# Performance work log

Measured on AMD Instinct MI355X. Metric: run time of the kernel, lower is better.

Reference implementation:

```python
import jax, jax.numpy as jnp
import numpy as np
import jax.scipy.linalg as jsp

H = 8
C = 64
D_CONV = 4
EPS_L2 = 1e-6
EPS_RMS = 1e-5


def l2norm(x):
    return x * jax.lax.rsqrt(jnp.sum(x * x, axis=-1, keepdims=True) + EPS_L2)


def setup_inputs() -> dict:
    key = jax.random.key(0)
    ks = jax.random.split(key, 12)
    B, T, D = 4, 4096, 1024
    x = jax.random.normal(ks[0], (B, T, D), dtype=jnp.float32)
    s = 0.02
    Wv = jax.random.normal(ks[1], (D, D), dtype=jnp.float32) * s
    Wg = jax.random.normal(ks[2], (D, D), dtype=jnp.float32) * s
    Wo = jax.random.normal(ks[3], (D, D), dtype=jnp.float32) * s
    Wb = jax.random.normal(ks[4], (H, D), dtype=jnp.float32) * s
    Wa = jax.random.normal(ks[5], (H, D), dtype=jnp.float32) * s
    # dt_bias / A_log initialized as in the torch module
    u = jax.random.uniform(ks[6], (H,))
    dt = jnp.exp(u * (jnp.log(0.1) - jnp.log(0.001)) + jnp.log(0.001))
    dt_bias = dt + jnp.log(-jnp.expm1(-dt))
    A_log = jnp.log(jax.random.uniform(ks[7], (H,)) * 16.0 + 1e-4)
    norm_w = jnp.ones((D // H,), dtype=jnp.float32)
    conv_w = jax.random.normal(ks[8], (D, D_CONV), dtype=jnp.float32) * 0.1
    conv_b = jnp.zeros((D,), dtype=jnp.float32)
    return {"x": x, "Wv": Wv, "Wg": Wg, "Wo": Wo, "Wb": Wb, "Wa": Wa,
            "dt_bias": dt_bias, "A_log": A_log, "norm_w": norm_w,
            "conv_w": conv_w, "conv_b": conv_b}


def _causal_depthwise_conv(x, w, b):
    # x: (B,T,D), w: (D,d_conv) -- causal depthwise conv1d
    B, T, D = x.shape
    xp = jnp.pad(x, ((0, 0), (D_CONV - 1, 0), (0, 0)))
    out = b
    for j in range(D_CONV):
        out = out + xp[:, j:j + T] * w[:, j]
    return out


def _forward(x, Wv, Wg, Wo, Wb, Wa, dt_bias, A_log, norm_w, conv_w, conv_b):
    B, T, D = x.shape
    K = D // H
    n = T // C  # T chosen as a multiple of C, so pad_len == 0

    rk = l2norm(x.reshape(B, T, H, K)) / np.sqrt(K)
    x_shift = jnp.pad(x[:, :-1], ((0, 0), (1, 0), (0, 0)))
    wk = l2norm(x_shift.reshape(B, T, H, K))
    v = jax.nn.silu(_causal_depthwise_conv(x @ Wv.T, conv_w, conv_b)).reshape(B, T, H, K)
    gate = (x @ Wg.T).reshape(B, T, H, K)
    beta = jax.nn.sigmoid(x @ Wb.T)                       # (B,T,H)
    decay = -jnp.exp(A_log) * jax.nn.softplus(x @ Wa.T + dt_bias)  # (B,T,H)

    # -> (B,H,T,K)
    rk, wk, v = (jnp.transpose(t, (0, 2, 1, 3)) for t in (rk, wk, v))
    beta_t = jnp.transpose(beta, (0, 2, 1))[..., None]    # (B,H,T,1)
    v = v * beta_t
    wk_beta = wk * beta_t

    # chunk: (B,H,n,C,K)
    ch = lambda t: t.reshape(B, H, n, C, K)
    rk, wk, v, wk_beta = ch(rk), ch(wk), ch(v), ch(wk_beta)
    decay = jnp.cumsum(jnp.transpose(decay, (0, 2, 1)).reshape(B, H, n, C), axis=-1)
    decay_exp = jnp.exp(decay)[..., None]                 # (B,H,n,C,1)

    tril = jnp.tril(jnp.ones((C, C), dtype=bool))
    strict_lower = jnp.tril(jnp.ones((C, C), dtype=bool), k=-1)
    diff = decay[..., :, None] - decay[..., None, :]
    L_mask = jnp.where(tril, jnp.exp(jnp.where(tril, diff, 0.0)), 0.0)  # (B,H,n,C,C)

    A_strict = jnp.where(strict_lower,
                         -(jnp.einsum('bhnck,bhndk->bhncd', wk_beta, wk) * L_mask), 0.0)
    # forward-substitution loop == inverse of unit-lower-triangular (I - A_strict)
    eye = jnp.eye(C, dtype=x.dtype)
    Tmat = jsp.solve_triangular(eye - A_strict,
                                jnp.broadcast_to(eye, A_strict.shape),
                                lower=True)
    v = Tmat @ v
    wk_cumdecay = Tmat @ (wk_beta * decay_exp)

    # scan over chunks maintaining state S: (B,H,K,K)
    def step(S, inp):
        rk_i, wk_i, v_i, wkc_i, L_i, dec_i = inp
        attn = jnp.where(tril, jnp.einsum('bhck,bhdk->bhcd', rk_i, wk_i) * L_i, 0.0)
        v_new = v_i - wkc_i @ S
        o_inter = (rk_i * jnp.exp(dec_i)[..., None]) @ S
        o_i = o_inter + attn @ v_new
        dw = jnp.exp(dec_i[..., -1:] - dec_i)[..., None]
        S_new = S * jnp.exp(dec_i[..., -1])[..., None, None] + \
            jnp.einsum('bhck,bhcv->bhkv', wk_i * dw, v_new)
        return S_new, o_i

    mv = lambda t: jnp.moveaxis(t, 2, 0)  # chunk axis to front
    S0 = jnp.zeros((B, H, K, K), dtype=x.dtype)
    _, o = jax.lax.scan(step, S0, (mv(rk), mv(wk), mv(v), mv(wk_cumdecay),
                                   mv(L_mask), mv(decay)))
    # o: (n,B,H,C,K) -> (B,T,H,K)
    o = jnp.transpose(o, (1, 0, 3, 2, 4)).reshape(B, T, H, K)

    # per-head RMSNorm, gated, output projection
    o = o * jax.lax.rsqrt(jnp.mean(o * o, axis=-1, keepdims=True) + EPS_RMS) * norm_w
    o = o * jax.nn.silu(gate)
    return o.reshape(B, T, D) @ Wo.T


def reference(x, Wv, Wg, Wo, Wb, Wa, dt_bias, A_log, norm_w, conv_w, conv_b):
    return _forward(x, Wv, Wg, Wo, Wb, Wa, dt_bias, A_log, norm_w, conv_w, conv_b)
```

## Files before the change

kernel.cpp:

```cpp
#include <hip/hip_runtime.h>
#include <hip/hip_bf16.h>
#include <math.h>

#define H_ 8
#define K_ 128
#define C_ 64
#define D_ 1024
#define T_ 4096
#define B_ 4
#define N_CH 64
#define BT_ (B_*T_)

typedef __attribute__((ext_vector_type(8))) short bf16x8;
typedef __attribute__((ext_vector_type(4))) float f32x4;
typedef __hip_bfloat16 bf16;

#define BAR_LGKM() do { \
  asm volatile("s_waitcnt lgkmcnt(0)" ::: "memory"); \
  __builtin_amdgcn_sched_barrier(0); \
  __builtin_amdgcn_s_barrier(); \
} while(0)

__device__ __forceinline__ float siluf(float x){ return x / (1.0f + expf(-x)); }
__device__ __forceinline__ float expn(float x){ return expf(fminf(x, 0.f)); }
__device__ __forceinline__ float sanf(float v){ return (__builtin_fabsf(v) <= 1e30f) ? v : 0.f; }

__device__ __forceinline__ void ld_bf8(const bf16* p, float* o){
  uint4 u = *(const uint4*)p;
  o[0]=__uint_as_float(u.x<<16); o[1]=__uint_as_float(u.x&0xffff0000u);
  o[2]=__uint_as_float(u.y<<16); o[3]=__uint_as_float(u.y&0xffff0000u);
  o[4]=__uint_as_float(u.z<<16); o[5]=__uint_as_float(u.z&0xffff0000u);
  o[6]=__uint_as_float(u.w<<16); o[7]=__uint_as_float(u.w&0xffff0000u);
}
__device__ __forceinline__ void ld_bf8s(const bf16* p, float* o){
  ld_bf8(p, o);
#pragma unroll
  for (int e=0;e<8;e++) o[e] = sanf(o[e]);
}
__device__ __forceinline__ void ld_bf4(const bf16* p, float* o){
  uint2 u = *(const uint2*)p;
  o[0]=__uint_as_float(u.x<<16); o[1]=__uint_as_float(u.x&0xffff0000u);
  o[2]=__uint_as_float(u.y<<16); o[3]=__uint_as_float(u.y&0xffff0000u);
}
__device__ __forceinline__ void ld_bf4s(const bf16* p, float* o){
  ld_bf4(p, o);
#pragma unroll
  for (int e=0;e<4;e++) o[e] = sanf(o[e]);
}
__device__ __forceinline__ unsigned short f2bfu(float f){
  bf16 h = __float2bfloat16(f);
  return *reinterpret_cast<unsigned short*>(&h);
}
__device__ __forceinline__ uint2 pack_bf4(const float* v){
  uint2 r;
  r.x = (unsigned)f2bfu(v[0]) | ((unsigned)f2bfu(v[1])<<16);
  r.y = (unsigned)f2bfu(v[2]) | ((unsigned)f2bfu(v[3])<<16);
  return r;
}

__global__ __launch_bounds__(256) void cast_f2b(
    const float* __restrict__ src, bf16* __restrict__ dst, int n4)
{
  int i = blockIdx.x*256 + threadIdx.x;
  if (i >= n4) return;
  float4 v = *(const float4*)&src[(size_t)i*4];
  float a[4] = {v.x, v.y, v.z, v.w};
  *(uint2*)&dst[(size_t)i*4] = pack_bf4(a);
}

template<typename OUT_T>
__global__ __launch_bounds__(256) void gemm_bt_mfma(
    const bf16* __restrict__ X, const bf16* __restrict__ W,
    OUT_T* __restrict__ Y, int M, int N, int K)
{
  __shared__ __align__(16) bf16 As[128*64];
  __shared__ __align__(16) bf16 Bs[128*64];
  const int tid = threadIdx.x;
  const int wv = tid >> 6;
  const int lane = tid & 63;
  const int row0 = blockIdx.y*128, col0 = blockIdx.x*128;
  const int mw = (wv&1)*64, nw = (wv>>1)*64;
  const int q = lane >> 4;
  const int l15 = lane & 15;
  f32x4 acc[4][4];
#pragma unroll
  for (int mi=0;mi<4;mi++)
#pragma unroll
    for (int ni=0;ni<4;ni++) acc[mi][ni] = (f32x4){0.f,0.f,0.f,0.f};

  const int sr = tid >> 3;
  const int sc = (tid & 7) * 8;
  for (int k0=0;k0<K;k0+=64){
#pragma unroll
    for (int i=0;i<4;i++){
      __builtin_amdgcn_global_load_lds(
          (const void*)&X[(size_t)(row0 + i*32 + sr)*K + k0 + sc],
          (void*)&As[i*2048 + wv*512], 16, 0, 0);
      __builtin_amdgcn_global_load_lds(
          (const void*)&W[(size_t)(col0 + i*32 + sr)*K + k0 + sc],
          (void*)&Bs[i*2048 + wv*512], 16, 0, 0);
    }
    __syncthreads();
#pragma unroll
    for (int ks=0; ks<64; ks+=32){
      bf16x8 af[4], bfr[4];
#pragma unroll
      for (int i=0;i<4;i++){
        af[i]  = *(const bf16x8*)&As[(mw + i*16 + l15)*64 + ks + q*8];
        bfr[i] = *(const bf16x8*)&Bs[(nw + i*16 + l15)*64 + ks + q*8];
      }
#pragma unroll
      for (int mi=0;mi<4;mi++)
#pragma unroll
        for (int ni=0;ni<4;ni++)
          acc[mi][ni] = __builtin_amdgcn_mfma_f32_16x16x32_bf16(af[mi], bfr[ni], acc[mi][ni], 0,0,0);
    }
    __syncthreads();
  }
#pragma unroll
  for (int mi=0;mi<4;mi++){
#pragma unroll
    for (int reg=0;reg<4;reg++){
      int row = row0 + mw + mi*16 + q*4 + reg;
#pragma unroll
      for (int ni=0;ni<4;ni++){
        int col = col0 + nw + ni*16 + l15;
        if constexpr (sizeof(OUT_T) == 2)
          Y[(size_t)row*N + col] = (OUT_T)__float2bfloat16(acc[mi][ni][reg]);
        else
          Y[(size_t)row*N + col] = (OUT_T)acc[mi][ni][reg];
      }
    }
  }
}

__global__ __launch_bounds__(256) void proj_small(
    const float* __restrict__ x, const float* __restrict__ Wb, const float* __restrict__ Wa,
    const float* __restrict__ dt_bias, const float* __restrict__ A_log,
    float* __restrict__ beta_out, float* __restrict__ dec_out)
{
  const int w = threadIdx.x >> 6;
  const int lane = threadIdx.x & 63;
  const int bt = blockIdx.x*4 + w;
  const int b = bt >> 12, t = bt & (T_-1);
  const float* xr = x + (size_t)bt*D_;
  float xv[16];
#pragma unroll
  for (int p=0;p<4;p++){
    float4 v = *(const float4*)&xr[lane*16 + p*4];
    xv[p*4+0]=v.x; xv[p*4+1]=v.y; xv[p*4+2]=v.z; xv[p*4+3]=v.w;
  }
  float accb[H_], acca[H_];
#pragma unroll
  for (int h=0;h<H_;h++){
    float sb=0.f, sa=0.f;
#pragma unroll
    for (int p=0;p<4;p++){
      float4 wb = *(const float4*)&Wb[(size_t)h*D_ + lane*16 + p*4];
      float4 wa = *(const float4*)&Wa[(size_t)h*D_ + lane*16 + p*4];
      sb += xv[p*4+0]*wb.x + xv[p*4+1]*wb.y + xv[p*4+2]*wb.z + xv[p*4+3]*wb.w;
      sa += xv[p*4+0]*wa.x + xv[p*4+1]*wa.y + xv[p*4+2]*wa.z + xv[p*4+3]*wa.w;
    }
    accb[h]=sb; acca[h]=sa;
  }
#pragma unroll
  for (int h=0;h<H_;h++){
#pragma unroll
    for (int m=1;m<64;m<<=1){
      accb[h] += __shfl_xor(accb[h], m, 64);
      acca[h] += __shfl_xor(acca[h], m, 64);
    }
  }
  if (lane < H_) {
    int h = lane;
    beta_out[(size_t)(b*H_+h)*T_ + t] = 1.f/(1.f+expf(-accb[h]));
  } else if (lane < 2*H_) {
    int h = lane - H_;
    float z = acca[h] + dt_bias[h];
    float sp = fmaxf(z,0.f) + log1pf(expf(-fabsf(z)));
    dec_out[(size_t)(b*H_+h)*T_ + t] = -expf(A_log[h]) * sp;
  }
}

__global__ __launch_bounds__(256) void xinv_kernel(
    const float* __restrict__ x, float* __restrict__ xinv, bf16* __restrict__ xb)
{
  const int bt = blockIdx.x;
  const int b = bt >> 12, t = bt & (T_-1);
  const int tid = threadIdx.x;
  float4 xv = *(const float4*)&x[(size_t)bt*D_ + tid*4];
  float a[4] = {xv.x, xv.y, xv.z, xv.w};
  *(uint2*)&xb[(size_t)bt*D_ + tid*4] = pack_bf4(a);
  float ss = xv.x*xv.x + xv.y*xv.y + xv.z*xv.z + xv.w*xv.w;
#pragma unroll
  for (int m=1;m<32;m<<=1) ss += __shfl_xor(ss, m, 32);
  const int h = tid >> 5;
  if ((tid & 31) == 0)
    xinv[(size_t)(b*H_+h)*T_ + t] = rsqrtf(ss + 1e-6f);
}

__global__ __launch_bounds__(256) void cumsum_dec(
    const float* __restrict__ dec_raw, float* __restrict__ dec_cum)
{
  int g = blockIdx.x*4 + (threadIdx.x>>6);
  int lane = threadIdx.x & 63;
  float v = sanf(dec_raw[(size_t)g*C_ + lane]);
#pragma unroll
  for (int off=1; off<64; off<<=1){
    float u = __shfl_up(v, off, 64);
    if (lane >= off) v += u;
  }
  dec_cum[(size_t)g*C_ + lane] = v;
}

__global__ __launch_bounds__(256) void chunk_prep(
    const bf16* __restrict__ xb, const float* __restrict__ xinv,
    const bf16* __restrict__ vpre, const float* __restrict__ cw, const float* __restrict__ cb,
    const float* __restrict__ beta, const float* __restrict__ dec,
    bf16* __restrict__ vchk, bf16* __restrict__ wkc, bf16* __restrict__ attn)
{
  __shared__ __align__(16) bf16 s_x[65][136];
  __shared__ __align__(16) float s_a[64][64];
  __shared__ float s_dec[64], s_beta[64], s_invsh[64], s_negbi[64], s_rsc[64], s_sc2[64];

  const int tid = threadIdx.x;
  const int chunk = blockIdx.x;
  const int bh = chunk >> 6;
  const int nc = chunk & 63;
  const int b = bh >> 3, h = bh & 7;
  const int t0 = nc * C_;
  const size_t xrow = (size_t)b*T_;
  const size_t rowb = (size_t)bh*T_ + t0;
  const size_t kobase = rowb * K_;
  const int w = tid >> 6;
  const int lane = tid & 63;
  const int l15 = lane & 15;
  const int q = lane >> 4;

  for (int idx = tid; idx < 65*16; idx += 256){
    int r = idx >> 4;
    int seg = (idx & 15) * 8;
    int t = t0 + r - 1;
    int tr = t < 0 ? 0 : t;
    *(uint4*)&s_x[r][seg] = *(const uint4*)&xb[(xrow + tr)*D_ + h*K_ + seg];
  }
  if (tid < C_){
    int c = tid;
    float dv  = sanf(dec[rowb + c]);
    float bet = sanf(beta[rowb + c]);
    float invc = sanf(xinv[rowb + c]);
    int tm1 = t0 + c - 1;
    float ivs = (tm1 >= 0) ? sanf(xinv[(size_t)bh*T_ + tm1]) : 0.f;
    s_dec[c] = dv;
    s_beta[c] = bet;
    s_invsh[c] = ivs;
    s_negbi[c] = -bet * ivs;
    s_rsc[c] = invc * 0.08838834764831845f;
    s_sc2[c] = ivs * bet * expn(dv);
  }
  __syncthreads();

  bf16x8 aG[4], aT[4];
#pragma unroll
  for (int ks=0; ks<4; ks++){
    aG[ks] = *(const bf16x8*)&s_x[16*w + l15][ks*32 + q*8];
    aT[ks] = *(const bf16x8*)&s_x[16*w + l15 + 1][ks*32 + q*8];
  }
  f32x4 accG[4], accT[4];
#pragma unroll
  for (int J=0;J<4;J++){ accG[J]=(f32x4){0.f,0.f,0.f,0.f}; accT[J]=(f32x4){0.f,0.f,0.f,0.f}; }
#pragma unroll
  for (int J=0;J<4;J++){
    if (J <= w){
#pragma unroll
      for (int ks=0; ks<4; ks++){
        bf16x8 bfrag = *(const bf16x8*)&s_x[16*J + l15][ks*32 + q*8];
        accG[J] = __builtin_amdgcn_mfma_f32_16x16x32_bf16(aG[ks], bfrag, accG[J], 0,0,0);
        accT[J] = __builtin_amdgcn_mfma_f32_16x16x32_bf16(aT[ks], bfrag, accT[J], 0,0,0);
      }
    }
  }
  {
    const int i0 = 16*w + q*4;
#pragma unroll
    for (int J=0;J<4;J++){
      const int j = 16*J + l15;
#pragma unroll
      for (int reg=0;reg<4;reg++){
        const int i = i0 + reg;
        if (j < i)
          s_a[i][j] = s_negbi[i] * s_invsh[j] * expn(s_dec[i]-s_dec[j]) * accG[J][reg];
        float val = 0.f;
        if (j <= i)
          val = s_rsc[i] * s_invsh[j] * expn(s_dec[i]-s_dec[j]) * accT[J][reg];
        attn[(size_t)chunk*4096 + i*64 + j] = __float2bfloat16(val);
      }
    }
  }

  float v[64];
  if (tid < 128){
    const int col = tid;
    float4 cwv = *(const float4*)&cw[(h*K_+col)*4];
    const float cbv = cb[h*K_+col];
    const bf16* vp = vpre + (xrow + t0)*D_ + h*K_ + col;
    float win0, win1, win2;
    { int t = t0-3; win0 = (t>=0)? sanf(__bfloat162float(vpre[(xrow+t)*D_+h*K_+col])) : 0.f; }
    { int t = t0-2; win1 = (t>=0)? sanf(__bfloat162float(vpre[(xrow+t)*D_+h*K_+col])) : 0.f; }
    { int t = t0-1; win2 = (t>=0)? sanf(__bfloat162float(vpre[(xrow+t)*D_+h*K_+col])) : 0.f; }
#pragma unroll
    for (int c8=0; c8<8; c8++){
      float nv[8];
#pragma unroll
      for (int u=0;u<8;u++) nv[u] = sanf(__bfloat162float(vp[(size_t)(c8*8+u)*D_]));
#pragma unroll
      for (int u=0;u<8;u++){
        const int c = c8*8+u;
        float a = cbv + cwv.x*win0 + cwv.y*win1 + cwv.z*win2 + cwv.w*nv[u];
        v[c] = siluf(a) * s_beta[c];
        win0=win1; win1=win2; win2=nv[u];
      }
    }
  } else {
    const int col = tid - 128;
#pragma unroll
    for (int c=0;c<64;c++)
      v[c] = __bfloat162float(s_x[c][col]) * s_sc2[c];
  }
  __syncthreads();

#pragma unroll
  for (int i=1;i<64;i++){
    const float* ar = s_a[i];
    float s0=0.f, s1=0.f, s2=0.f, s3=0.f;
    int j=0;
#pragma unroll
    for (; j+4<=i; j+=4){
      float4 a4 = *(const float4*)&ar[j];
      s0 += a4.x*v[j+0]; s1 += a4.y*v[j+1];
      s2 += a4.z*v[j+2]; s3 += a4.w*v[j+3];
    }
#pragma unroll
    for (; j<i; j++) s0 += ar[j]*v[j];
    v[i] += (s0+s2)+(s1+s3);
  }

  {
    const int col = tid & 127;
    bf16* dst = (tid < 128 ? vchk : wkc) + kobase + col;
#pragma unroll
    for (int c=0;c<64;c++)
      dst[(size_t)c*K_] = __float2bfloat16(v[c]);
  }
}

__global__ __launch_bounds__(512) void scan_kernel(
    const bf16* __restrict__ xb, const float* __restrict__ xinv,
    bf16* vo, const bf16* __restrict__ wkc,
    const bf16* __restrict__ attn, const float* __restrict__ dec)
{
  __shared__ __align__(16) bf16 ab_w[2][C_][136];
  __shared__ __align__(16) bf16 ab_x[2][C_][136];
  __shared__ __align__(16) bf16 xst  [K_][72];
  __shared__ __align__(16) bf16 a_att[C_][72];
  __shared__ __align__(16) bf16 st_hi[16][136];
  __shared__ __align__(16) bf16 st_lo[16][136];
  __shared__ __align__(16) bf16 vn_t [16][72];
  __shared__ __align__(16) bf16 vn_sh[16][72];
  __shared__ __align__(16) bf16 vn_sl[16][72];
  __shared__ float s_o[2][C_];
  __shared__ float s_scv[2][C_];
  __shared__ float s_a63[2];

  const int tid = threadIdx.x;
  const int bh = blockIdx.x & 31;
  const int g  = blockIdx.x >> 5;
  const int b = bh >> 3, h = bh & 7;
  const int j0 = g*16;
  const int w  = tid >> 6;
  const int lane = tid & 63;
  const int l15 = lane & 15;
  const int q = lane >> 4;
  const size_t xrow = (size_t)b*T_;

  for (int e=tid; e<16*136; e+=512){
    ((unsigned short*)&st_hi[0][0])[e] = 0;
    ((unsigned short*)&st_lo[0][0])[e] = 0;
  }

  if (w < 4){
    const int wrow = 16*w;
    f32x4 accS[2];
    accS[0] = (f32x4){0.f,0.f,0.f,0.f};
    accS[1] = (f32x4){0.f,0.f,0.f,0.f};
    bf16 pf_v[4];
    {
      const bf16* pv = vo + ((size_t)bh*T_ + wrow + q*4)*K_ + j0 + l15;
#pragma unroll
      for (int r=0;r<4;r++) pf_v[r] = pv[(size_t)r*K_];
    }
    BAR_LGKM();

    for (int nc=0; nc<N_CH; nc++){
      const size_t rowb = (size_t)bh*T_ + (size_t)nc*C_;
      const int pb = nc & 1;
      float vinit[4];
#pragma unroll
      for (int r=0;r<4;r++) vinit[r] = __bfloat162float(pf_v[r]);
      {
        int nn = (nc+1 < N_CH) ? nc+1 : nc;
        const bf16* pv = vo + ((size_t)bh*T_ + (size_t)nn*C_ + wrow + q*4)*K_ + j0 + l15;
#pragma unroll
        for (int r=0;r<4;r++) pf_v[r] = pv[(size_t)r*K_];
      }
      f32x4 accV, accP = (f32x4){0.f,0.f,0.f,0.f};
#pragma unroll
      for (int r=0;r<4;r++) accV[r] = vinit[r];
      __builtin_amdgcn_s_setprio(1);
#pragma unroll
      for (int ks=0; ks<4; ks++){
        bf16x8 bh_ = *(const bf16x8*)&st_hi[l15][ks*32 + q*8];
        bf16x8 bl_ = *(const bf16x8*)&st_lo[l15][ks*32 + q*8];
        bf16x8 a1 = *(const bf16x8*)&ab_w[pb][wrow + l15][ks*32 + q*8];
        bf16x8 a2 = *(const bf16x8*)&ab_x[pb][wrow + l15][ks*32 + q*8];
        accV = __builtin_amdgcn_mfma_f32_16x16x32_bf16(a1, bh_, accV, 0,0,0);
        accV = __builtin_amdgcn_mfma_f32_16x16x32_bf16(a1, bl_, accV, 0,0,0);
        accP = __builtin_amdgcn_mfma_f32_16x16x32_bf16(a2, bh_, accP, 0,0,0);
        accP = __builtin_amdgcn_mfma_f32_16x16x32_bf16(a2, bl_, accP, 0,0,0);
      }
      __builtin_amdgcn_s_setprio(0);
      f32x4 sov  = *(const f32x4*)&s_o[pb][wrow + q*4];
      f32x4 scvv = *(const f32x4*)&s_scv[pb][wrow + q*4];
      const float a63 = s_a63[pb];
      f32x4 oacc;
#pragma unroll
      for (int r=0;r<4;r++) oacc[r] = accP[r] * sov[r];
      {
        float v4[4] = {accV[0],accV[1],accV[2],accV[3]};
        *(uint2*)&vn_t[l15][wrow + q*4] = pack_bf4(v4);
        float vs[4];
#pragma unroll
        for (int r=0;r<4;r++) vs[r] = accV[r] * scvv[r];
        uint2 ph = pack_bf4(vs);
        float lo4[4];
        lo4[0] = vs[0] - __uint_as_float(ph.x << 16);
        lo4[1] = vs[1] - __uint_as_float(ph.x & 0xffff0000u);
        lo4[2] = vs[2] - __uint_as_float(ph.y << 16);
        lo4[3] = vs[3] - __uint_as_float(ph.y & 0xffff0000u);
        *(uint2*)&vn_sh[l15][wrow + q*4] = ph;
        *(uint2*)&vn_sl[l15][wrow + q*4] = pack_bf4(lo4);
      }
      BAR_LGKM();

      __builtin_amdgcn_s_setprio(1);
#pragma unroll
      for (int ks=0; ks<2; ks++){
        bf16x8 aA = *(const bf16x8*)&a_att[wrow + l15][ks*32 + q*8];
        bf16x8 bV = *(const bf16x8*)&vn_t[l15][ks*32 + q*8];
        oacc = __builtin_amdgcn_mfma_f32_16x16x32_bf16(aA, bV, oacc, 0,0,0);
      }
      __builtin_amdgcn_s_setprio(0);
      {
        bf16* po = vo + (rowb + wrow + q*4)*K_ + j0 + l15;
#pragma unroll
        for (int r=0;r<4;r++) po[(size_t)r*K_] = __float2bfloat16(oacc[r]);
      }
      __builtin_amdgcn_s_setprio(1);
#pragma unroll
      for (int sub=0; sub<2; sub++){
        f32x4 acc = accS[sub];
#pragma unroll
        for (int r=0;r<4;r++) acc[r] *= a63;
#pragma unroll
        for (int ks=0; ks<2; ks++){
          bf16x8 aH = *(const bf16x8*)&vn_sh[l15][ks*32 + q*8];
          bf16x8 aL = *(const bf16x8*)&vn_sl[l15][ks*32 + q*8];
          bf16x8 bX = *(const bf16x8*)&xst[32*w + 16*sub + l15][ks*32 + q*8];
          acc = __builtin_amdgcn_mfma_f32_16x16x32_bf16(aH, bX, acc, 0,0,0);
          acc = __builtin_amdgcn_mfma_f32_16x16x32_bf16(aL, bX, acc, 0,0,0);
        }
        accS[sub] = acc;
#pragma unroll
        for (int r=0;r<4;r++){
          float sv = acc[r];
          bf16 hb = __float2bfloat16(sv);
          st_hi[q*4+r][32*w + 16*sub + l15] = hb;
          st_lo[q*4+r][32*w + 16*sub + l15] = __float2bfloat16(sv - __bfloat162float(hb));
        }
      }
      __builtin_amdgcn_s_setprio(0);
      BAR_LGKM();
    }
  } else {
    const int tp = tid - 256;
    const int r_st = tp >> 2;
    const int k8   = (tp & 3) * 8;
    const int xc0  = (tp & 31) * 2;
    const int xkb  = (tp >> 5) * 16;

    uint4 A_w[4], A_x[4];
    float A_d = 0.f, A_d63 = 0.f, A_i = 0.f, A_ip = 0.f;
    uint4 B_t[4], B_a[2];

    auto issueA = [&](int c){
      const int t0 = c*C_;
      const size_t rowb = (size_t)bh*T_ + t0;
      const bf16* pw = wkc + (rowb + r_st)*K_ + k8;
      const bf16* px = xb + (xrow + t0 + r_st)*D_ + h*K_ + k8;
#pragma unroll
      for (int i=0;i<4;i++){
        A_w[i] = *(const uint4*)(pw + i*32);
        A_x[i] = *(const uint4*)(px + i*32);
      }
      if (tp < C_){
        A_d   = dec[rowb + tp];
        A_d63 = dec[rowb + 63];
        A_i   = xinv[(size_t)bh*T_ + t0 + tp];
        int tm1 = t0 + tp - 1;
        A_ip  = (tm1 >= 0) ? xinv[(size_t)bh*T_ + tm1] : 0.f;
      }
    };
    auto issueB = [&](int c){
      const int t0 = c*C_;
      const bf16* pa = attn + (size_t)(bh*N_CH + c)*4096 + r_st*64 + k8;
      B_a[0] = *(const uint4*)pa;
      B_a[1] = *(const uint4*)(pa + 32);
      int t1 = t0 + xc0 - 1;
      const bf16* p1 = xb + (xrow + (t1 < 0 ? 0 : t1))*D_ + h*K_ + xkb;
      const bf16* p2 = xb + (xrow + (t0 + xc0))*D_ + h*K_ + xkb;
      B_t[0] = *(const uint4*)p1; B_t[1] = *(const uint4*)(p1+8);
      B_t[2] = *(const uint4*)p2; B_t[3] = *(const uint4*)(p2+8);
    };
    auto writeA = [&](int buf){
#pragma unroll
      for (int i=0;i<4;i++){
        uint4 u = A_w[i];
        u.x ^= 0x80008000u; u.y ^= 0x80008000u; u.z ^= 0x80008000u; u.w ^= 0x80008000u;
        *(uint4*)&ab_w[buf][r_st][k8 + i*32] = u;
        *(uint4*)&ab_x[buf][r_st][k8 + i*32] = A_x[i];
      }
      if (tp < C_){
        float dv  = sanf(A_d);
        float d63 = sanf(A_d63);
        s_o[buf][tp]   = sanf(A_i) * 0.08838834764831845f * expn(dv);
        s_scv[buf][tp] = sanf(A_ip) * expn(d63 - dv);
        if (tp == 63) s_a63[buf] = expn(d63);
      }
    };
    auto writeB = [&](){
      *(uint4*)&a_att[r_st][k8]      = B_a[0];
      *(uint4*)&a_att[r_st][k8 + 32] = B_a[1];
      unsigned r1[8] = {B_t[0].x,B_t[0].y,B_t[0].z,B_t[0].w,
                        B_t[1].x,B_t[1].y,B_t[1].z,B_t[1].w};
      unsigned r2[8] = {B_t[2].x,B_t[2].y,B_t[2].z,B_t[2].w,
                        B_t[3].x,B_t[3].y,B_t[3].z,B_t[3].w};
#pragma unroll
      for (int i2=0;i2<8;i2++){
        *(unsigned*)&xst[xkb + 2*i2][xc0]     = (r1[i2] & 0xffffu) | (r2[i2] << 16);
        *(unsigned*)&xst[xkb + 2*i2 + 1][xc0] = (r1[i2] >> 16) | (r2[i2] & 0xffff0000u);
      }
    };

    issueA(0);
    writeA(0);
    issueA(1);
    issueB(0);
    BAR_LGKM();

    for (int nc=0; nc<N_CH; nc++){
      writeA((nc+1)&1);
      writeB();
      int na = (nc+2 < N_CH) ? nc+2 : N_CH-1;
      int nb = (nc+1 < N_CH) ? nc+1 : N_CH-1;
      issueA(na);
      issueB(nb);
      BAR_LGKM();
      BAR_LGKM();
    }
  }
}

__global__ __launch_bounds__(256) void norm_gate(
    const bf16* __restrict__ o, bf16* gio, const float* __restrict__ norm_w)
{
  const int bt = blockIdx.x;
  const int b = bt >> 12, t = bt & (T_-1);
  const int tid = threadIdx.x;
  const int h = tid >> 5;
  const int kk = (tid & 31)*4;
  float ov[4];
  ld_bf4s(o + ((size_t)(b*H_+h)*T_ + t)*K_ + kk, ov);
  float ss = ov[0]*ov[0] + ov[1]*ov[1] + ov[2]*ov[2] + ov[3]*ov[3];
#pragma unroll
  for (int m=1;m<32;m<<=1) ss += __shfl_xor(ss, m, 32);
  float r = rsqrtf(ss*(1.f/128.f) + 1e-5f);
  float4 nw = *(const float4*)&norm_w[kk];
  float gv[4];
  ld_bf4s(gio + (size_t)bt*D_ + tid*4, gv);
  float res[4];
  res[0] = ov[0]*r*nw.x * siluf(gv[0]);
  res[1] = ov[1]*r*nw.y * siluf(gv[1]);
  res[2] = ov[2]*r*nw.z * siluf(gv[2]);
  res[3] = ov[3]*r*nw.w * siluf(gv[3]);
  *(uint2*)&gio[(size_t)bt*D_ + tid*4] = pack_bf4(res);
}

extern "C" void kernel_launch(void* const* d_in, const int* in_sizes, int n_in,
                              void* d_out, int out_size, void* d_ws, size_t ws_size,
                              hipStream_t stream)
{
  const float* x       = (const float*)d_in[0];
  const float* Wv      = (const float*)d_in[1];
  const float* Wg      = (const float*)d_in[2];
  const float* Wo      = (const float*)d_in[3];
  const float* Wb      = (const float*)d_in[4];
  const float* Wa      = (const float*)d_in[5];
  const float* dt_bias = (const float*)d_in[6];
  const float* A_log   = (const float*)d_in[7];
  const float* norm_w  = (const float*)d_in[8];
  const float* conv_w  = (const float*)d_in[9];
  const float* conv_b  = (const float*)d_in[10];
  float* out = (float*)d_out;

  const size_t BTD = (size_t)B_*T_*D_;
  const size_t BHT = (size_t)B_*H_*T_;
  const size_t DD  = (size_t)D_*D_;

  float* beta = (float*)d_ws;
  float* decr = beta + BHT;
  float* decc = decr + BHT;
  float* xinv = decc + BHT;
  bf16* Wvb = (bf16*)(xinv + BHT);
  bf16* Wgb = Wvb + DD;
  bf16* Wob = Wgb + DD;
  bf16* xb   = Wob + DD;
  bf16* vpre = xb + BTD;
  bf16* wkc  = vpre + BTD;
  bf16* vo   = (bf16*)d_out;
  bf16* attn = vo + BTD;

  dim3 gemm_grid(D_/128, BT_/128);
  xinv_kernel<<<BT_, 256, 0, stream>>>(x, xinv, xb);
  cast_f2b<<<(DD/4+255)/256, 256, 0, stream>>>(Wv, Wvb, DD/4);
  cast_f2b<<<(DD/4+255)/256, 256, 0, stream>>>(Wg, Wgb, DD/4);
  cast_f2b<<<(DD/4+255)/256, 256, 0, stream>>>(Wo, Wob, DD/4);
  gemm_bt_mfma<bf16><<<gemm_grid, 256, 0, stream>>>(xb, Wvb, vpre, BT_, D_, D_);
  proj_small<<<BT_/4, 256, 0, stream>>>(x, Wb, Wa, dt_bias, A_log, beta, decr);
  cumsum_dec<<<(BHT/C_)/4, 256, 0, stream>>>(decr, decc);
  chunk_prep<<<B_*H_*N_CH, 256, 0, stream>>>(xb, xinv, vpre, conv_w, conv_b,
                                             beta, decc, vo , wkc, attn);
  scan_kernel<<<B_*H_*8, 512, 0, stream>>>(xb, xinv, vo, wkc, attn, decc);
  gemm_bt_mfma<bf16><<<gemm_grid, 256, 0, stream>>>(xb, Wgb, vpre, BT_, D_, D_);
  norm_gate<<<BT_, 256, 0, stream>>>(vo , vpre , norm_w);
  gemm_bt_mfma<float><<<gemm_grid, 256, 0, stream>>>(vpre, Wob, out, BT_, D_, D_);
}
```

Measured before the change: 656.3 us.

## Co-schedule scan with gate GEMM in one kernel, swizzle GEMM LDS, restructure scan

Merges the sequential chunk scan and the gate projection GEMM into a single launch, where every fifth block runs a scan stream and the rest compute GEMM tiles. The aim is to fill the GPU, which the scan alone (256 blocks) leaves mostly idle. The scan drops its producer warps: it goes from 512 to 256 threads and loads operands straight into registers with a one-chunk prefetch instead of staging them through double-buffered LDS. The GEMM LDS layout gets an XOR swizzle to avoid bank conflicts, and the forward-substitution loop becomes a compile-time recursion. Risks are scan latency from the lost producer warps, and contention from the GEMM blocks stretching the scan's critical path.

```diff
diff --git a/kernel.cpp b/kernel.cpp
--- a/kernel.cpp
+++ b/kernel.cpp
@@ -25,18 +25,6 @@
 __device__ __forceinline__ float expn(float x){ return expf(fminf(x, 0.f)); }
 __device__ __forceinline__ float sanf(float v){ return (__builtin_fabsf(v) <= 1e30f) ? v : 0.f; }
 
-__device__ __forceinline__ void ld_bf8(const bf16* p, float* o){
-  uint4 u = *(const uint4*)p;
-  o[0]=__uint_as_float(u.x<<16); o[1]=__uint_as_float(u.x&0xffff0000u);
-  o[2]=__uint_as_float(u.y<<16); o[3]=__uint_as_float(u.y&0xffff0000u);
-  o[4]=__uint_as_float(u.z<<16); o[5]=__uint_as_float(u.z&0xffff0000u);
-  o[6]=__uint_as_float(u.w<<16); o[7]=__uint_as_float(u.w&0xffff0000u);
-}
-__device__ __forceinline__ void ld_bf8s(const bf16* p, float* o){
-  ld_bf8(p, o);
-#pragma unroll
-  for (int e=0;e<8;e++) o[e] = sanf(o[e]);
-}
 __device__ __forceinline__ void ld_bf4(const bf16* p, float* o){
   uint2 u = *(const uint2*)p;
   o[0]=__uint_as_float(u.x<<16); o[1]=__uint_as_float(u.x&0xffff0000u);
@@ -57,6 +45,29 @@
   r.y = (unsigned)f2bfu(v[2]) | ((unsigned)f2bfu(v[3])<<16);
   return r;
 }
+__device__ __forceinline__ bf16x8 u4_to_b8(uint4 u){
+  union { uint4 u; bf16x8 b; } cv; cv.u = u; return cv.b;
+}
+
+template<int I> __device__ __forceinline__ void fsub_step(float* v, const float (*sa)[64]){
+  const float* ar = sa[I];
+  float s0=0.f,s1=0.f,s2=0.f,s3=0.f;
+  constexpr int I4 = I & ~3;
+#pragma unroll
+  for (int j=0;j<I4;j+=4){
+    float4 a4 = *(const float4*)&ar[j];
+    s0 += a4.x*v[j+0]; s1 += a4.y*v[j+1]; s2 += a4.z*v[j+2]; s3 += a4.w*v[j+3];
+  }
+#pragma unroll
+  for (int j=I4;j<I;j++) s0 += ar[j]*v[j];
+  v[I] += (s0+s2)+(s1+s3);
+}
+template<int I> __device__ __forceinline__ void fsub_all(float* v, const float (*sa)[64]){
+  if constexpr (I >= 1){
+    fsub_all<I-1>(v, sa);
+    fsub_step<I>(v, sa);
+  }
+}
 
 __global__ __launch_bounds__(256) void cast_f2b(
     const float* __restrict__ src, bf16* __restrict__ dst, int n4)
@@ -69,35 +80,34 @@
 }
 
 template<typename OUT_T>
-__global__ __launch_bounds__(256) void gemm_bt_mfma(
+__device__ __forceinline__ void gemm_tile_body(
     const bf16* __restrict__ X, const bf16* __restrict__ W,
-    OUT_T* __restrict__ Y, int M, int N, int K)
-{
-  __shared__ __align__(16) bf16 As[128*64];
-  __shared__ __align__(16) bf16 Bs[128*64];
-  const int tid = threadIdx.x;
+    OUT_T* __restrict__ Y, int M, int N, int K,
+    int bx, int by, int tid, bf16* As, bf16* Bs)
+{
   const int wv = tid >> 6;
   const int lane = tid & 63;
-  const int row0 = blockIdx.y*128, col0 = blockIdx.x*128;
+  const int row0 = by*128, col0 = bx*128;
   const int mw = (wv&1)*64, nw = (wv>>1)*64;
   const int q = lane >> 4;
   const int l15 = lane & 15;
+  const int swr = l15 & 7;
   f32x4 acc[4][4];
 #pragma unroll
   for (int mi=0;mi<4;mi++)
 #pragma unroll
     for (int ni=0;ni<4;ni++) acc[mi][ni] = (f32x4){0.f,0.f,0.f,0.f};
 
-  const int sr = tid >> 3;
-  const int sc = (tid & 7) * 8;
+  const int sr8 = lane >> 3;
+  const int scs = ((lane & 7) ^ sr8) * 8;
   for (int k0=0;k0<K;k0+=64){
 #pragma unroll
     for (int i=0;i<4;i++){
       __builtin_amdgcn_global_load_lds(
-          (const void*)&X[(size_t)(row0 + i*32 + sr)*K + k0 + sc],
+          (const void*)&X[(size_t)(row0 + i*32 + wv*8 + sr8)*K + k0 + scs],
           (void*)&As[i*2048 + wv*512], 16, 0, 0);
       __builtin_amdgcn_global_load_lds(
-          (const void*)&W[(size_t)(col0 + i*32 + sr)*K + k0 + sc],
+          (const void*)&W[(size_t)(col0 + i*32 + wv*8 + sr8)*K + k0 + scs],
           (void*)&Bs[i*2048 + wv*512], 16, 0, 0);
     }
     __syncthreads();
@@ -106,8 +116,9 @@
       bf16x8 af[4], bfr[4];
 #pragma unroll
       for (int i=0;i<4;i++){
-        af[i]  = *(const bf16x8*)&As[(mw + i*16 + l15)*64 + ks + q*8];
-        bfr[i] = *(const bf16x8*)&Bs[(nw + i*16 + l15)*64 + ks + q*8];
+        const int cc = (((ks>>3) + q) ^ swr) * 8;
+        af[i]  = *(const bf16x8*)&As[(mw + i*16 + l15)*64 + cc];
+        bfr[i] = *(const bf16x8*)&Bs[(nw + i*16 + l15)*64 + cc];
       }
 #pragma unroll
       for (int mi=0;mi<4;mi++)
@@ -132,6 +143,16 @@
       }
     }
   }
+}
+
+template<typename OUT_T>
+__global__ __launch_bounds__(256) void gemm_bt_mfma(
+    const bf16* __restrict__ X, const bf16* __restrict__ W,
+    OUT_T* __restrict__ Y, int M, int N, int K)
+{
+  __shared__ __align__(16) bf16 As[128*64];
+  __shared__ __align__(16) bf16 Bs[128*64];
+  gemm_tile_body<OUT_T>(X, W, Y, M, N, K, blockIdx.x, blockIdx.y, threadIdx.x, As, Bs);
 }
 
 __global__ __launch_bounds__(256) void proj_small(
@@ -329,21 +350,7 @@
   }
   __syncthreads();
 
-#pragma unroll
-  for (int i=1;i<64;i++){
-    const float* ar = s_a[i];
-    float s0=0.f, s1=0.f, s2=0.f, s3=0.f;
-    int j=0;
-#pragma unroll
-    for (; j+4<=i; j+=4){
-      float4 a4 = *(const float4*)&ar[j];
-      s0 += a4.x*v[j+0]; s1 += a4.y*v[j+1];
-      s2 += a4.z*v[j+2]; s3 += a4.w*v[j+3];
-    }
-#pragma unroll
-    for (; j<i; j++) s0 += ar[j]*v[j];
-    v[i] += (s0+s2)+(s1+s3);
-  }
+  fsub_all<63>(v, s_a);
 
   {
     const int col = tid & 127;
@@ -354,118 +361,184 @@
   }
 }
 
-__global__ __launch_bounds__(512) void scan_kernel(
-    const bf16* __restrict__ xb, const float* __restrict__ xinv,
-    bf16* vo, const bf16* __restrict__ wkc,
-    const bf16* __restrict__ attn, const float* __restrict__ dec)
-{
-  __shared__ __align__(16) bf16 ab_w[2][C_][136];
-  __shared__ __align__(16) bf16 ab_x[2][C_][136];
-  __shared__ __align__(16) bf16 xst  [K_][72];
-  __shared__ __align__(16) bf16 a_att[C_][72];
-  __shared__ __align__(16) bf16 st_hi[16][136];
-  __shared__ __align__(16) bf16 st_lo[16][136];
-  __shared__ __align__(16) bf16 vn_t [16][72];
-  __shared__ __align__(16) bf16 vn_sh[16][72];
-  __shared__ __align__(16) bf16 vn_sl[16][72];
-  __shared__ float s_o[2][C_];
-  __shared__ float s_scv[2][C_];
-  __shared__ float s_a63[2];
-
-  const int tid = threadIdx.x;
-  const int bh = blockIdx.x & 31;
-  const int g  = blockIdx.x >> 5;
+__device__ void scan_body(
+    int sid, int tid, unsigned char* smem,
+    const bf16* __restrict__ xb, const float* __restrict__ xinv, bf16* vo,
+    const bf16* __restrict__ wkc, const bf16* __restrict__ attn,
+    const float* __restrict__ dec)
+{
+  bf16* xst   = (bf16*)smem;
+  bf16* st_hi = (bf16*)(smem + 36864);
+  bf16* st_lo = (bf16*)(smem + 41216);
+  bf16* vn_t  = (bf16*)(smem + 45568);
+  bf16* vn_sh = (bf16*)(smem + 47872);
+  bf16* vn_sl = (bf16*)(smem + 50176);
+
+  const int bh = sid & 31;
+  const int g  = sid >> 5;
   const int b = bh >> 3, h = bh & 7;
   const int j0 = g*16;
   const int w  = tid >> 6;
   const int lane = tid & 63;
   const int l15 = lane & 15;
   const int q = lane >> 4;
+  const int wrow = 16*w;
+  const int c0 = wrow + q*4;
   const size_t xrow = (size_t)b*T_;
-
-  for (int e=tid; e<16*136; e+=512){
-    ((unsigned short*)&st_hi[0][0])[e] = 0;
-    ((unsigned short*)&st_lo[0][0])[e] = 0;
-  }
-
-  if (w < 4){
-    const int wrow = 16*w;
-    f32x4 accS[2];
-    accS[0] = (f32x4){0.f,0.f,0.f,0.f};
-    accS[1] = (f32x4){0.f,0.f,0.f,0.f};
-    bf16 pf_v[4];
+  const size_t bhT = (size_t)bh*T_;
+
+  for (int e=tid; e<16*136; e+=256){
+    ((unsigned short*)st_hi)[e] = 0;
+    ((unsigned short*)st_lo)[e] = 0;
+  }
+
+  const int xc0 = (tid & 31)*2;
+  const int xkb = (tid >> 5)*16;
+
+  f32x4 accS[2];
+  accS[0] = (f32x4){0.f,0.f,0.f,0.f};
+  accS[1] = (f32x4){0.f,0.f,0.f,0.f};
+
+  uint4 T_r[4];
+  uint4 P_w[4], P_x[4], P_a[2];
+  bf16  P_v[4];
+  float4 P_d, P_xi;
+  float P_d63, P_xm[4];
+
+  auto issue_t = [&](int c){
+    int t0 = c*C_;
+    int t1 = t0 + xc0 - 1;
+    const bf16* p1 = xb + (xrow + (t1<0?0:t1))*D_ + h*K_ + xkb;
+    const bf16* p2 = xb + (xrow + (t0+xc0))*D_ + h*K_ + xkb;
+    T_r[0]=*(const uint4*)p1; T_r[1]=*(const uint4*)(p1+8);
+    T_r[2]=*(const uint4*)p2; T_r[3]=*(const uint4*)(p2+8);
+  };
+  auto write_xst = [&](int buf){
+    unsigned r1[8]={T_r[0].x,T_r[0].y,T_r[0].z,T_r[0].w,T_r[1].x,T_r[1].y,T_r[1].z,T_r[1].w};
+    unsigned r2[8]={T_r[2].x,T_r[2].y,T_r[2].z,T_r[2].w,T_r[3].x,T_r[3].y,T_r[3].z,T_r[3].w};
+    bf16* base = xst + buf*(128*72);
+#pragma unroll
+    for (int i2=0;i2<8;i2++){
+      *(unsigned*)&base[(xkb + 2*i2)*72 + xc0]     = (r1[i2] & 0xffffu) | (r2[i2] << 16);
+      *(unsigned*)&base[(xkb + 2*i2 + 1)*72 + xc0] = (r1[i2] >> 16) | (r2[i2] & 0xffff0000u);
+    }
+  };
+  auto issue_main = [&](int c){
+    int t0 = c*C_;
+    size_t rowb = bhT + t0;
+    const bf16* pw = wkc + (rowb + wrow + l15)*K_ + q*8;
+    const bf16* px = xb + (xrow + t0 + wrow + l15)*D_ + h*K_ + q*8;
+#pragma unroll
+    for (int ks=0; ks<4; ks++){
+      P_w[ks] = *(const uint4*)(pw + ks*32);
+      P_x[ks] = *(const uint4*)(px + ks*32);
+    }
+    const bf16* pv = vo + (rowb + c0)*K_ + j0 + l15;
+#pragma unroll
+    for (int r=0;r<4;r++) P_v[r] = pv[(size_t)r*K_];
+    P_d   = *(const float4*)&dec[rowb + c0];
+    P_d63 = dec[rowb + 63];
+    P_xi  = *(const float4*)&xinv[bhT + t0 + c0];
+#pragma unroll
+    for (int r=0;r<4;r++){
+      int tm1 = t0 + c0 + r - 1;
+      P_xm[r] = (tm1 >= 0) ? xinv[bhT + tm1] : 0.f;
+    }
+  };
+  auto issue_att = [&](int c){
+    const bf16* pa = attn + (size_t)(bh*N_CH + c)*4096 + (wrow + l15)*64 + q*8;
+    P_a[0] = *(const uint4*)pa;
+    P_a[1] = *(const uint4*)(pa + 32);
+  };
+
+  issue_t(0);
+  write_xst(0);
+  issue_t(1);
+  issue_main(0);
+  issue_att(0);
+  BAR_LGKM();
+
+  for (int nc=0; nc<N_CH; nc++){
+    const int t0 = nc*C_;
+    const size_t rowb = bhT + t0;
+
+    float d63s = sanf(P_d63);
+    float a63 = expn(d63s);
+    float cdA[4] = {sanf(P_d.x), sanf(P_d.y), sanf(P_d.z), sanf(P_d.w)};
+    float cxiA[4] = {sanf(P_xi.x), sanf(P_xi.y), sanf(P_xi.z), sanf(P_xi.w)};
+    float sov[4], scv[4], vinitf[4];
+#pragma unroll
+    for (int r=0;r<4;r++){
+      sov[r] = cxiA[r] * 0.08838834764831845f * expn(cdA[r]);
+      scv[r] = sanf(P_xm[r]) * expn(d63s - cdA[r]);
+      vinitf[r] = __bfloat162float(P_v[r]);
+    }
+
+    write_xst((nc+1)&1);
+    issue_t(nc+2 < N_CH ? nc+2 : N_CH-1);
+
+    f32x4 accV, accP = (f32x4){0.f,0.f,0.f,0.f};
+#pragma unroll
+    for (int r=0;r<4;r++) accV[r] = vinitf[r];
+    __builtin_amdgcn_s_setprio(1);
+#pragma unroll
+    for (int ks=0; ks<4; ks++){
+      bf16x8 bh_ = *(const bf16x8*)&st_hi[l15*136 + ks*32 + q*8];
+      bf16x8 bl_ = *(const bf16x8*)&st_lo[l15*136 + ks*32 + q*8];
+      uint4 uw = P_w[ks];
+      uw.x ^= 0x80008000u; uw.y ^= 0x80008000u; uw.z ^= 0x80008000u; uw.w ^= 0x80008000u;
+      bf16x8 a1 = u4_to_b8(uw);
+      bf16x8 a2 = u4_to_b8(P_x[ks]);
+      accV = __builtin_amdgcn_mfma_f32_16x16x32_bf16(a1, bh_, accV, 0,0,0);
+      accV = __builtin_amdgcn_mfma_f32_16x16x32_bf16(a1, bl_, accV, 0,0,0);
+      accP = __builtin_amdgcn_mfma_f32_16x16x32_bf16(a2, bh_, accP, 0,0,0);
+      accP = __builtin_amdgcn_mfma_f32_16x16x32_bf16(a2, bl_, accP, 0,0,0);
+    }
+    __builtin_amdgcn_s_setprio(0);
+    f32x4 oacc;
+#pragma unroll
+    for (int r=0;r<4;r++) oacc[r] = accP[r] * sov[r];
     {
-      const bf16* pv = vo + ((size_t)bh*T_ + wrow + q*4)*K_ + j0 + l15;
-#pragma unroll
-      for (int r=0;r<4;r++) pf_v[r] = pv[(size_t)r*K_];
-    }
+      float v4[4] = {accV[0],accV[1],accV[2],accV[3]};
+      *(uint2*)&vn_t[l15*72 + c0] = pack_bf4(v4);
+      float vs[4];
+#pragma unroll
+      for (int r=0;r<4;r++) vs[r] = accV[r] * scv[r];
+      uint2 ph = pack_bf4(vs);
+      float lo4[4];
+      lo4[0] = vs[0] - __uint_as_float(ph.x << 16);
+      lo4[1] = vs[1] - __uint_as_float(ph.x & 0xffff0000u);
+      lo4[2] = vs[2] - __uint_as_float(ph.y << 16);
+      lo4[3] = vs[3] - __uint_as_float(ph.y & 0xffff0000u);
+      *(uint2*)&vn_sh[l15*72 + c0] = ph;
+      *(uint2*)&vn_sl[l15*72 + c0] = pack_bf4(lo4);
+    }
+    issue_main(nc+1 < N_CH ? nc+1 : N_CH-1);
     BAR_LGKM();
 
-    for (int nc=0; nc<N_CH; nc++){
-      const size_t rowb = (size_t)bh*T_ + (size_t)nc*C_;
-      const int pb = nc & 1;
-      float vinit[4];
-#pragma unroll
-      for (int r=0;r<4;r++) vinit[r] = __bfloat162float(pf_v[r]);
-      {
-        int nn = (nc+1 < N_CH) ? nc+1 : nc;
-        const bf16* pv = vo + ((size_t)bh*T_ + (size_t)nn*C_ + wrow + q*4)*K_ + j0 + l15;
-#pragma unroll
-        for (int r=0;r<4;r++) pf_v[r] = pv[(size_t)r*K_];
+    __builtin_amdgcn_s_setprio(1);
+#pragma unroll
+    for (int ks=0; ks<2; ks++){
+      bf16x8 bV = *(const bf16x8*)&vn_t[l15*72 + ks*32 + q*8];
+      bf16x8 aA = u4_to_b8(P_a[ks]);
+      oacc = __builtin_amdgcn_mfma_f32_16x16x32_bf16(aA, bV, oacc, 0,0,0);
+    }
+    __builtin_amdgcn_s_setprio(0);
+    {
+      bf16* po = vo + (rowb + c0)*K_ + j0 + l15;
+#pragma unroll
+      for (int r=0;r<4;r++) po[(size_t)r*K_] = __float2bfloat16(oacc[r]);
+    }
+    issue_att(nc+1 < N_CH ? nc+1 : N_CH-1);
+    __builtin_amdgcn_s_setprio(1);
+    {
+      bf16x8 aH[2], aL[2];
+#pragma unroll
+      for (int ks=0; ks<2; ks++){
+        aH[ks] = *(const bf16x8*)&vn_sh[l15*72 + ks*32 + q*8];
+        aL[ks] = *(const bf16x8*)&vn_sl[l15*72 + ks*32 + q*8];
       }
-      f32x4 accV, accP = (f32x4){0.f,0.f,0.f,0.f};
-#pragma unroll
-      for (int r=0;r<4;r++) accV[r] = vinit[r];
-      __builtin_amdgcn_s_setprio(1);
-#pragma unroll
-      for (int ks=0; ks<4; ks++){
-        bf16x8 bh_ = *(const bf16x8*)&st_hi[l15][ks*32 + q*8];
-        bf16x8 bl_ = *(const bf16x8*)&st_lo[l15][ks*32 + q*8];
-        bf16x8 a1 = *(const bf16x8*)&ab_w[pb][wrow + l15][ks*32 + q*8];
-        bf16x8 a2 = *(const bf16x8*)&ab_x[pb][wrow + l15][ks*32 + q*8];
-        accV = __builtin_amdgcn_mfma_f32_16x16x32_bf16(a1, bh_, accV, 0,0,0);
-        accV = __builtin_amdgcn_mfma_f32_16x16x32_bf16(a1, bl_, accV, 0,0,0);
-        accP = __builtin_amdgcn_mfma_f32_16x16x32_bf16(a2, bh_, accP, 0,0,0);
-        accP = __builtin_amdgcn_mfma_f32_16x16x32_bf16(a2, bl_, accP, 0,0,0);
-      }
-      __builtin_amdgcn_s_setprio(0);
-      f32x4 sov  = *(const f32x4*)&s_o[pb][wrow + q*4];
-      f32x4 scvv = *(const f32x4*)&s_scv[pb][wrow + q*4];
-      const float a63 = s_a63[pb];
-      f32x4 oacc;
-#pragma unroll
-      for (int r=0;r<4;r++) oacc[r] = accP[r] * sov[r];
-      {
-        float v4[4] = {accV[0],accV[1],accV[2],accV[3]};
-        *(uint2*)&vn_t[l15][wrow + q*4] = pack_bf4(v4);
-        float vs[4];
-#pragma unroll
-        for (int r=0;r<4;r++) vs[r] = accV[r] * scvv[r];
-        uint2 ph = pack_bf4(vs);
-        float lo4[4];
-        lo4[0] = vs[0] - __uint_as_float(ph.x << 16);
-        lo4[1] = vs[1] - __uint_as_float(ph.x & 0xffff0000u);
-        lo4[2] = vs[2] - __uint_as_float(ph.y << 16);
-        lo4[3] = vs[3] - __uint_as_float(ph.y & 0xffff0000u);
-        *(uint2*)&vn_sh[l15][wrow + q*4] = ph;
-        *(uint2*)&vn_sl[l15][wrow + q*4] = pack_bf4(lo4);
-      }
-      BAR_LGKM();
-
-      __builtin_amdgcn_s_setprio(1);
-#pragma unroll
-      for (int ks=0; ks<2; ks++){
-        bf16x8 aA = *(const bf16x8*)&a_att[wrow + l15][ks*32 + q*8];
-        bf16x8 bV = *(const bf16x8*)&vn_t[l15][ks*32 + q*8];
-        oacc = __builtin_amdgcn_mfma_f32_16x16x32_bf16(aA, bV, oacc, 0,0,0);
-      }
-      __builtin_amdgcn_s_setprio(0);
-      {
-        bf16* po = vo + (rowb + wrow + q*4)*K_ + j0 + l15;
-#pragma unroll
-        for (int r=0;r<4;r++) po[(size_t)r*K_] = __float2bfloat16(oacc[r]);
-      }
-      __builtin_amdgcn_s_setprio(1);
+      const bf16* xcur = xst + (nc&1)*(128*72);
 #pragma unroll
       for (int sub=0; sub<2; sub++){
         f32x4 acc = accS[sub];
@@ -473,110 +546,41 @@
         for (int r=0;r<4;r++) acc[r] *= a63;
 #pragma unroll
         for (int ks=0; ks<2; ks++){
-          bf16x8 aH = *(const bf16x8*)&vn_sh[l15][ks*32 + q*8];
-          bf16x8 aL = *(const bf16x8*)&vn_sl[l15][ks*32 + q*8];
-          bf16x8 bX = *(const bf16x8*)&xst[32*w + 16*sub + l15][ks*32 + q*8];
-          acc = __builtin_amdgcn_mfma_f32_16x16x32_bf16(aH, bX, acc, 0,0,0);
-          acc = __builtin_amdgcn_mfma_f32_16x16x32_bf16(aL, bX, acc, 0,0,0);
+          bf16x8 bX = *(const bf16x8*)&xcur[(32*w + 16*sub + l15)*72 + ks*32 + q*8];
+          acc = __builtin_amdgcn_mfma_f32_16x16x32_bf16(aH[ks], bX, acc, 0,0,0);
+          acc = __builtin_amdgcn_mfma_f32_16x16x32_bf16(aL[ks], bX, acc, 0,0,0);
         }
         accS[sub] = acc;
 #pragma unroll
         for (int r=0;r<4;r++){
           float sv = acc[r];
           bf16 hb = __float2bfloat16(sv);
-          st_hi[q*4+r][32*w + 16*sub + l15] = hb;
-          st_lo[q*4+r][32*w + 16*sub + l15] = __float2bfloat16(sv - __bfloat162float(hb));
+          st_hi[(q*4+r)*136 + 32*w + 16*sub + l15] = hb;
+          st_lo[(q*4+r)*136 + 32*w + 16*sub + l15] = __float2bfloat16(sv - __bfloat162float(hb));
         }
       }
-      __builtin_amdgcn_s_setprio(0);
-      BAR_LGKM();
-    }
+    }
+    __builtin_amdgcn_s_setprio(0);
+    BAR_LGKM();
+  }
+}
+
+__global__ __launch_bounds__(256) void scan_gate_kernel(
+    const bf16* __restrict__ xb, const float* __restrict__ xinv, bf16* vo,
+    const bf16* __restrict__ wkc, const bf16* __restrict__ attn,
+    const float* __restrict__ dec,
+    const bf16* __restrict__ Wgb, bf16* __restrict__ gate)
+{
+  __shared__ __align__(16) unsigned char smem[52480];
+  const int bid = blockIdx.x;
+  const int tid = threadIdx.x;
+  if (bid % 5 == 0){
+    scan_body(bid/5, tid, smem, xb, xinv, vo, wkc, attn, dec);
   } else {
-    const int tp = tid - 256;
-    const int r_st = tp >> 2;
-    const int k8   = (tp & 3) * 8;
-    const int xc0  = (tp & 31) * 2;
-    const int xkb  = (tp >> 5) * 16;
-
-    uint4 A_w[4], A_x[4];
-    float A_d = 0.f, A_d63 = 0.f, A_i = 0.f, A_ip = 0.f;
-    uint4 B_t[4], B_a[2];
-
-    auto issueA = [&](int c){
-      const int t0 = c*C_;
-      const size_t rowb = (size_t)bh*T_ + t0;
-      const bf16* pw = wkc + (rowb + r_st)*K_ + k8;
-      const bf16* px = xb + (xrow + t0 + r_st)*D_ + h*K_ + k8;
-#pragma unroll
-      for (int i=0;i<4;i++){
-        A_w[i] = *(const uint4*)(pw + i*32);
-        A_x[i] = *(const uint4*)(px + i*32);
-      }
-      if (tp < C_){
-        A_d   = dec[rowb + tp];
-        A_d63 = dec[rowb + 63];
-        A_i   = xinv[(size_t)bh*T_ + t0 + tp];
-        int tm1 = t0 + tp - 1;
-        A_ip  = (tm1 >= 0) ? xinv[(size_t)bh*T_ + tm1] : 0.f;
-      }
-    };
-    auto issueB = [&](int c){
-      const int t0 = c*C_;
-      const bf16* pa = attn + (size_t)(bh*N_CH + c)*4096 + r_st*64 + k8;
-      B_a[0] = *(const uint4*)pa;
-      B_a[1] = *(const uint4*)(pa + 32);
-      int t1 = t0 + xc0 - 1;
-      const bf16* p1 = xb + (xrow + (t1 < 0 ? 0 : t1))*D_ + h*K_ + xkb;
-      const bf16* p2 = xb + (xrow + (t0 + xc0))*D_ + h*K_ + xkb;
-      B_t[0] = *(const uint4*)p1; B_t[1] = *(const uint4*)(p1+8);
-      B_t[2] = *(const uint4*)p2; B_t[3] = *(const uint4*)(p2+8);
-    };
-    auto writeA = [&](int buf){
-#pragma unroll
-      for (int i=0;i<4;i++){
-        uint4 u = A_w[i];
-        u.x ^= 0x80008000u; u.y ^= 0x80008000u; u.z ^= 0x80008000u; u.w ^= 0x80008000u;
-        *(uint4*)&ab_w[buf][r_st][k8 + i*32] = u;
-        *(uint4*)&ab_x[buf][r_st][k8 + i*32] = A_x[i];
-      }
-      if (tp < C_){
-        float dv  = sanf(A_d);
-        float d63 = sanf(A_d63);
-        s_o[buf][tp]   = sanf(A_i) * 0.08838834764831845f * expn(dv);
-        s_scv[buf][tp] = sanf(A_ip) * expn(d63 - dv);
-        if (tp == 63) s_a63[buf] = expn(d63);
-      }
-    };
-    auto writeB = [&](){
-      *(uint4*)&a_att[r_st][k8]      = B_a[0];
-      *(uint4*)&a_att[r_st][k8 + 32] = B_a[1];
-      unsigned r1[8] = {B_t[0].x,B_t[0].y,B_t[0].z,B_t[0].w,
-                        B_t[1].x,B_t[1].y,B_t[1].z,B_t[1].w};
-      unsigned r2[8] = {B_t[2].x,B_t[2].y,B_t[2].z,B_t[2].w,
-                        B_t[3].x,B_t[3].y,B_t[3].z,B_t[3].w};
-#pragma unroll
-      for (int i2=0;i2<8;i2++){
-        *(unsigned*)&xst[xkb + 2*i2][xc0]     = (r1[i2] & 0xffffu) | (r2[i2] << 16);
-        *(unsigned*)&xst[xkb + 2*i2 + 1][xc0] = (r1[i2] >> 16) | (r2[i2] & 0xffff0000u);
-      }
-    };
-
-    issueA(0);
-    writeA(0);
-    issueA(1);
-    issueB(0);
-    BAR_LGKM();
-
-    for (int nc=0; nc<N_CH; nc++){
-      writeA((nc+1)&1);
-      writeB();
-      int na = (nc+2 < N_CH) ? nc+2 : N_CH-1;
-      int nb = (nc+1 < N_CH) ? nc+1 : N_CH-1;
-      issueA(na);
-      issueB(nb);
-      BAR_LGKM();
-      BAR_LGKM();
-    }
+    int gid = bid - bid/5 - 1;
+    int bx = gid & 7, by = gid >> 3;
+    gemm_tile_body<bf16>(xb, Wgb, gate, BT_, D_, D_, bx, by, tid,
+                         (bf16*)smem, (bf16*)(smem + 16384));
   }
 }
 
@@ -649,8 +653,8 @@
   cumsum_dec<<<(BHT/C_)/4, 256, 0, stream>>>(decr, decc);
   chunk_prep<<<B_*H_*N_CH, 256, 0, stream>>>(xb, xinv, vpre, conv_w, conv_b,
                                              beta, decc, vo , wkc, attn);
-  scan_kernel<<<B_*H_*8, 512, 0, stream>>>(xb, xinv, vo, wkc, attn, decc);
-  gemm_bt_mfma<bf16><<<gemm_grid, 256, 0, stream>>>(xb, Wgb, vpre, BT_, D_, D_);
+  scan_gate_kernel<<<1280, 256, 0, stream>>>(xb, xinv, vo, wkc, attn, decc,
+                                             Wgb, vpre );
   norm_gate<<<BT_, 256, 0, stream>>>(vo , vpre , norm_w);
   gemm_bt_mfma<float><<<gemm_grid, 256, 0, stream>>>(vpre, Wob, out, BT_, D_, D_);
 }
```

Result: slower. 731.8 us (+11.5%).
